# Performance work log

Measured on AMD Instinct MI355X. Metric: run time of the kernel, lower is better.

## Reference

```python
import jax, jax.numpy as jnp
import numpy as np

N_NODES = 50000
N_EDGES = 800000
VOCAB = 1000
EMBED = 128
HIDDEN = 128
N_CLASSES = 10
N_GRAPHS = 64


def setup_inputs() -> dict:
    key = jax.random.key(0)
    ks = jax.random.split(key, 12)
    x_idx = jax.random.randint(ks[0], (N_NODES,), 0, VOCAB)
    edge_index = jax.random.randint(ks[1], (2, N_EDGES), 0, N_NODES)
    batch = jnp.sort(jax.random.randint(ks[2], (N_NODES,), 0, N_GRAPHS))
    s = lambda k, shp, fan: jax.random.normal(k, shp, jnp.float32) / jnp.sqrt(fan)
    return {
        "x_idx": x_idx,
        "edge_index": edge_index,
        "batch": batch,
        "embed_table": jax.random.normal(ks[3], (VOCAB, EMBED), jnp.float32),
        "Wl1": s(ks[4], (HIDDEN, EMBED), EMBED),
        "bl1": jnp.zeros((HIDDEN,), jnp.float32),
        "Wr1": s(ks[5], (HIDDEN, EMBED), EMBED),
        "Wl2": s(ks[6], (HIDDEN, HIDDEN), HIDDEN),
        "bl2": jnp.zeros((HIDDEN,), jnp.float32),
        "Wr2": s(ks[7], (HIDDEN, HIDDEN), HIDDEN),
        "linW": s(ks[8], (N_CLASSES, HIDDEN), HIDDEN),
        "linb": jnp.zeros((N_CLASSES,), jnp.float32),
    }


def _sage_conv(x, src, dst, Wl, bl, Wr):
    # mean aggregation of source features into destination nodes (PyG SAGEConv, aggr='mean')
    msg_sum = jax.ops.segment_sum(x[src], dst, num_segments=N_NODES)  # [N, d]
    cnt = jax.ops.segment_sum(jnp.ones((src.shape[0],), x.dtype), dst, num_segments=N_NODES)
    agg = msg_sum / jnp.maximum(cnt, 1.0)[:, None]
    # out = lin_l(agg) + lin_r(x); lin_l has bias, lin_r has none
    return agg @ Wl.T + bl + x @ Wr.T


def reference(x_idx, edge_index, batch, embed_table, Wl1, bl1, Wr1, Wl2, bl2, Wr2, linW, linb):
    src, dst = edge_index[0], edge_index[1]
    x = embed_table[x_idx]  # [N, EMBED]
    x = jax.nn.relu(_sage_conv(x, src, dst, Wl1, bl1, Wr1))
    x = jax.nn.relu(_sage_conv(x, src, dst, Wl2, bl2, Wr2))
    # global mean pool over graphs
    g_sum = jax.ops.segment_sum(x, batch, num_segments=N_GRAPHS)  # [G, HIDDEN]
    g_cnt = jax.ops.segment_sum(jnp.ones((x.shape[0],), x.dtype), batch, num_segments=N_GRAPHS)
    pooled = g_sum / jnp.maximum(g_cnt, 1.0)[:, None]
    return pooled @ linW.T + linb  # [G, N_CLASSES]
```

## Files before the change

### kernel.cpp

```cpp
#include <hip/hip_runtime.h>

#define N_NODES 50000
#define N_EDGES 800000
#define N_GRAPHS 64
#define SCAN_BLOCKS 196

#define NCHUNK 32
#define CHUNK_E (N_EDGES / NCHUNK)
#define NRANGE 4
#define RSZ (N_NODES / NRANGE)

#define K1_HIST (NCHUNK * NRANGE)
#define K1_EMBED (N_NODES * 16 / 256)
#define K1_PREP 32

#define QDW (N_NODES * 16)
#define QUS (N_NODES * 32)

typedef __bf16 bf16x8 __attribute__((ext_vector_type(8)));
typedef float f32x4 __attribute__((ext_vector_type(4)));

static __device__ __forceinline__ unsigned short f2bf(float f) {
    union { float f; unsigned u; } v; v.f = f;
    unsigned u = v.u;
    u += 0x7fffu + ((u >> 16) & 1u);
    return (unsigned short)(u >> 16);
}
static __device__ __forceinline__ float bf2f(unsigned short h) {
    union { unsigned u; float f; } v; v.u = ((unsigned)h) << 16; return v.f;
}
static __device__ __forceinline__ float bflo(unsigned w) {
    union { unsigned u; float f; } v; v.u = w << 16; return v.f;
}
static __device__ __forceinline__ float bfhi(unsigned w) {
    union { unsigned u; float f; } v; v.u = w & 0xffff0000u; return v.f;
}

__global__ __launch_bounds__(256) void k1_kernel(const int* __restrict__ dst,
                                                 int* __restrict__ part,
                                                 const int* __restrict__ x_idx,
                                                 const float* __restrict__ table,
                                                 unsigned short* __restrict__ X,
                                                 const float* __restrict__ Wl1,
                                                 const float* __restrict__ Wr1,
                                                 const float* __restrict__ Wl2,
                                                 const float* __restrict__ Wr2,
                                                 unsigned short* __restrict__ blob,
                                                 float* __restrict__ gsum) {
    const int b = blockIdx.x;
    if (b < K1_HIST) {
        __shared__ int h[RSZ];
        const int c = b >> 2;
        const int r = b & 3;
        const int rbase = r * RSZ;
        for (int i = threadIdx.x; i < RSZ; i += 256) h[i] = 0;
        __syncthreads();
        const int4* d4 = (const int4*)(dst + c * CHUNK_E);
        for (int i = threadIdx.x; i < CHUNK_E / 4; i += 256) {
            int4 d = d4[i];
            unsigned a;
            a = (unsigned)(d.x - rbase); if (a < RSZ) atomicAdd(&h[a], 1);
            a = (unsigned)(d.y - rbase); if (a < RSZ) atomicAdd(&h[a], 1);
            a = (unsigned)(d.z - rbase); if (a < RSZ) atomicAdd(&h[a], 1);
            a = (unsigned)(d.w - rbase); if (a < RSZ) atomicAdd(&h[a], 1);
        }
        __syncthreads();
        int* p = part + (size_t)c * N_NODES + rbase;
        for (int i = threadIdx.x; i < RSZ; i += 256) p[i] = h[i];
    } else if (b < K1_HIST + K1_EMBED) {
        int i = (b - K1_HIST) * 256 + threadIdx.x;
        int n = i >> 4, cq = i & 15;
        const float4* src = (const float4*)(table + (size_t)x_idx[n] * 128 + cq * 8);
        float4 a = src[0], bb = src[1];
        uint4 o;
        o.x = (unsigned)f2bf(a.x)  | ((unsigned)f2bf(a.y)  << 16);
        o.y = (unsigned)f2bf(a.z)  | ((unsigned)f2bf(a.w)  << 16);
        o.z = (unsigned)f2bf(bb.x) | ((unsigned)f2bf(bb.y) << 16);
        o.w = (unsigned)f2bf(bb.z) | ((unsigned)f2bf(bb.w) << 16);
        int qq = cq >> 2;
        ((uint4*)X)[(size_t)qq * (N_NODES * 4) + n * 4 + (cq & 3)] = o;
    } else {
        int s = (b - K1_HIST - K1_EMBED) * 256 + threadIdx.x;
        gsum[s] = 0.f;
        int g = s >> 12;
        int sl = s & 4095;
        int fidx = sl >> 6, lane = sl & 63;
        int m = fidx >> 5, kk = (fidx >> 3) & 3, tile = fidx & 7;
        const float* W = g ? (m ? Wr2 : Wl2) : (m ? Wr1 : Wl1);
        int n  = tile * 16 + (lane & 15);
        int k0 = kk * 32 + (lane >> 4) * 8;
        const float4* src = (const float4*)(W + n * 128 + k0);
        float4 a = src[0], bb = src[1];
        uint4 o;
        o.x = (unsigned)f2bf(a.x)  | ((unsigned)f2bf(a.y)  << 16);
        o.y = (unsigned)f2bf(a.z)  | ((unsigned)f2bf(a.w)  << 16);
        o.z = (unsigned)f2bf(bb.x) | ((unsigned)f2bf(bb.y) << 16);
        o.w = (unsigned)f2bf(bb.z) | ((unsigned)f2bf(bb.w) << 16);
        ((uint4*)blob)[s] = o;
    }
}

__global__ __launch_bounds__(256) void cntsum_kernel(const int* __restrict__ part,
                                                     int* __restrict__ cnt,
                                                     int* __restrict__ bsum) {
    int t = threadIdx.x;
    int n = blockIdx.x * 256 + t;
    int s = 0;
    if (n < N_NODES) {
#pragma unroll
        for (int c = 0; c < NCHUNK; ++c) s += part[(size_t)c * N_NODES + n];
        cnt[n] = s;
    }
#pragma unroll
    for (int off = 32; off > 0; off >>= 1) s += __shfl_down(s, off, 64);
    __shared__ int ws[4];
    if ((t & 63) == 0) ws[t >> 6] = s;
    __syncthreads();
    if (t == 0) bsum[blockIdx.x] = ws[0] + ws[1] + ws[2] + ws[3];
}

__global__ __launch_bounds__(256) void rowptroff_kernel(const int* __restrict__ cnt,
                                                        const int* __restrict__ bsum,
                                                        const int* __restrict__ part,
                                                        int* __restrict__ rowptr,
                                                        int* __restrict__ off) {
    __shared__ int sb[256];
    __shared__ int sd[256];
    int t = threadIdx.x;
    sb[t] = (t < SCAN_BLOCKS) ? bsum[t] : 0;
    __syncthreads();
    for (int o = 1; o < 256; o <<= 1) {
        int add = (t >= o) ? sb[t - o] : 0;
        __syncthreads();
        sb[t] += add;
        __syncthreads();
    }
    int boff = (blockIdx.x > 0) ? sb[blockIdx.x - 1] : 0;

    int i = blockIdx.x * 256 + t;
    int v = (i < N_NODES) ? cnt[i] : 0;
    sd[t] = v;
    __syncthreads();
    for (int o = 1; o < 256; o <<= 1) {
        int add = (t >= o) ? sd[t - o] : 0;
        __syncthreads();
        sd[t] += add;
        __syncthreads();
    }
    int excl = sd[t] - v + boff;
    if (i < N_NODES) {
        rowptr[i] = excl;
        if (i == N_NODES - 1) rowptr[N_NODES] = excl + v;
        int run = excl;
#pragma unroll
        for (int c = 0; c < NCHUNK; ++c) {
            off[(size_t)c * N_NODES + i] = run;
            run += part[(size_t)c * N_NODES + i];
        }
    }
}

__global__ __launch_bounds__(256) void scatter_kernel(const int* __restrict__ src,
                                                      const int* __restrict__ dst,
                                                      const int* __restrict__ off,
                                                      int* __restrict__ csr) {
    __shared__ int h[RSZ];
    const int c = blockIdx.x >> 2;
    const int r = blockIdx.x & 3;
    const int rbase = r * RSZ;
    const int* o = off + (size_t)c * N_NODES + rbase;
    for (int i = threadIdx.x; i < RSZ; i += 256) h[i] = o[i];
    __syncthreads();
    const int4* d4 = (const int4*)(dst + c * CHUNK_E);
    const int4* s4 = (const int4*)(src + c * CHUNK_E);
    for (int i = threadIdx.x; i < CHUNK_E / 4; i += 256) {
        int4 d = d4[i];
        int4 s = s4[i];
        unsigned a;
        a = (unsigned)(d.x - rbase); if (a < RSZ) csr[atomicAdd(&h[a], 1)] = s.x;
        a = (unsigned)(d.y - rbase); if (a < RSZ) csr[atomicAdd(&h[a], 1)] = s.y;
        a = (unsigned)(d.z - rbase); if (a < RSZ) csr[atomicAdd(&h[a], 1)] = s.z;
        a = (unsigned)(d.w - rbase); if (a < RSZ) csr[atomicAdd(&h[a], 1)] = s.w;
    }
}

__global__ __launch_bounds__(256) void agg_kernel(const unsigned* __restrict__ Xq,
                                                  const int* __restrict__ rowptr,
                                                  const int* __restrict__ csr,
                                                  unsigned* __restrict__ AGGq) {
    const int t = threadIdx.x;
    const int lane = t & 63;
    const int g = lane >> 4;
    const int f = lane & 15;
    const int n = blockIdx.x * 16 + (t >> 6) * 4 + g;
    const unsigned* Xb = Xq + (size_t)blockIdx.y * QDW;
    int beg = rowptr[n], end = rowptr[n + 1];
    float sx = 0.f, sy = 0.f;
    int i = beg;
    for (; i + 4 <= end; i += 4) {
        int s0 = csr[i], s1 = csr[i + 1], s2 = csr[i + 2], s3 = csr[i + 3];
        unsigned v0 = Xb[(size_t)s0 * 16 + f];
        unsigned v1 = Xb[(size_t)s1 * 16 + f];
        unsigned v2 = Xb[(size_t)s2 * 16 + f];
        unsigned v3 = Xb[(size_t)s3 * 16 + f];
        sx += (bflo(v0) + bflo(v1)) + (bflo(v2) + bflo(v3));
        sy += (bfhi(v0) + bfhi(v1)) + (bfhi(v2) + bfhi(v3));
    }
    for (; i < end; ++i) {
        unsigned v = Xb[(size_t)csr[i] * 16 + f];
        sx += bflo(v); sy += bfhi(v);
    }
    float inv = 1.f / (float)max(end - beg, 1);
    AGGq[(size_t)blockIdx.y * QDW + (size_t)n * 16 + f] =
        (unsigned)f2bf(sx * inv) | ((unsigned)f2bf(sy * inv) << 16);
}

__global__ __launch_bounds__(256) void gemm_kernel(const unsigned short* __restrict__ A0,
                                                   const unsigned short* __restrict__ A1,
                                                   const unsigned short* __restrict__ wblob,
                                                   const float* __restrict__ bias,
                                                   unsigned short* __restrict__ Y) {
    __shared__ char lds[65536];
    const int t = threadIdx.x, lane = t & 63, w = t >> 6;
    const int row0 = blockIdx.x * 128 + w * 32;

    {
        const char* src = (const char*)wblob + w * 16384 + lane * 16;
        char* dst = lds + w * 16384;
#pragma unroll
        for (int i = 0; i < 16; ++i) {
            __builtin_amdgcn_global_load_lds(
                (const __attribute__((address_space(1))) unsigned*)(src + i * 1024),
                (__attribute__((address_space(3))) unsigned*)(dst + i * 1024), 16, 0, 0);
        }
    }
    __syncthreads();

    f32x4 acc[2][8];
#pragma unroll
    for (int rt = 0; rt < 2; ++rt)
#pragma unroll
        for (int tl = 0; tl < 8; ++tl) acc[rt][tl] = (f32x4){0.f, 0.f, 0.f, 0.f};

    int rA = min(row0 + (lane & 15),      N_NODES - 1);
    int rB = min(row0 + 16 + (lane & 15), N_NODES - 1);
    const int kl = (lane >> 4) * 8;

#pragma unroll
    for (int km = 0; km < 8; ++km) {
        const unsigned short* Aq = ((km < 4) ? A0 : A1) + (size_t)(km & 3) * QUS;
        bf16x8 a0 = *(const bf16x8*)(Aq + (size_t)rA * 32 + kl);
        bf16x8 a1 = *(const bf16x8*)(Aq + (size_t)rB * 32 + kl);
        const char* bbase = lds + km * 8192 + lane * 16;
#pragma unroll
        for (int tile = 0; tile < 8; ++tile) {
            bf16x8 b = *(const bf16x8*)(bbase + tile * 1024);
            acc[0][tile] = __builtin_amdgcn_mfma_f32_16x16x32_bf16(a0, b, acc[0][tile], 0, 0, 0);
            acc[1][tile] = __builtin_amdgcn_mfma_f32_16x16x32_bf16(a1, b, acc[1][tile], 0, 0, 0);
        }
    }

    const int c     = lane & 15;
    const int rbase = (lane >> 4) * 4;
#pragma unroll
    for (int rt = 0; rt < 2; ++rt) {
#pragma unroll
        for (int tile = 0; tile < 8; ++tile) {
            int col = tile * 16 + c;
            float bv = bias[col];
            int q = col >> 5, wc = col & 31;
#pragma unroll
            for (int j = 0; j < 4; ++j) {
                int r = row0 + rt * 16 + rbase + j;
                if (r < N_NODES)
                    Y[(size_t)q * QUS + (size_t)r * 32 + wc] =
                        f2bf(fmaxf(acc[rt][tile][j] + bv, 0.f));
            }
        }
    }
}

__global__ __launch_bounds__(256) void gemm_pool_kernel(const unsigned short* __restrict__ A0,
                                                        const unsigned short* __restrict__ A1,
                                                        const unsigned short* __restrict__ wblob,
                                                        const float* __restrict__ bias,
                                                        const int* __restrict__ batch,
                                                        float* __restrict__ gsum) {
    __shared__ char lds[65536];
    const int t = threadIdx.x, lane = t & 63, w = t >> 6;
    const int brow0 = blockIdx.x * 128;
    const int row0  = brow0 + w * 32;

    {
        const char* src = (const char*)wblob + w * 16384 + lane * 16;
        char* dst = lds + w * 16384;
#pragma unroll
        for (int i = 0; i < 16; ++i) {
            __builtin_amdgcn_global_load_lds(
                (const __attribute__((address_space(1))) unsigned*)(src + i * 1024),
                (__attribute__((address_space(3))) unsigned*)(dst + i * 1024), 16, 0, 0);
        }
    }
    __syncthreads();

    f32x4 acc[2][8];
#pragma unroll
    for (int rt = 0; rt < 2; ++rt)
#pragma unroll
        for (int tl = 0; tl < 8; ++tl) acc[rt][tl] = (f32x4){0.f, 0.f, 0.f, 0.f};

    int rA = min(row0 + (lane & 15),      N_NODES - 1);
    int rB = min(row0 + 16 + (lane & 15), N_NODES - 1);
    const int kl = (lane >> 4) * 8;

#pragma unroll
    for (int km = 0; km < 8; ++km) {
        const unsigned short* Aq = ((km < 4) ? A0 : A1) + (size_t)(km & 3) * QUS;
        bf16x8 a0 = *(const bf16x8*)(Aq + (size_t)rA * 32 + kl);
        bf16x8 a1 = *(const bf16x8*)(Aq + (size_t)rB * 32 + kl);
        const char* bbase = lds + km * 8192 + lane * 16;
#pragma unroll
        for (int tile = 0; tile < 8; ++tile) {
            bf16x8 b = *(const bf16x8*)(bbase + tile * 1024);
            acc[0][tile] = __builtin_amdgcn_mfma_f32_16x16x32_bf16(a0, b, acc[0][tile], 0, 0, 0);
            acc[1][tile] = __builtin_amdgcn_mfma_f32_16x16x32_bf16(a1, b, acc[1][tile], 0, 0, 0);
        }
    }

    __syncthreads();
    float* ftile = (float*)lds;
    const int c     = lane & 15;
    const int rbase = (lane >> 4) * 4;
#pragma unroll
    for (int rt = 0; rt < 2; ++rt) {
#pragma unroll
        for (int tile = 0; tile < 8; ++tile) {
            int col = tile * 16 + c;
            float bv = bias[col];
#pragma unroll
            for (int j = 0; j < 4; ++j) {
                int lr = w * 32 + rt * 16 + rbase + j;
                ftile[lr * 128 + col] = fmaxf(acc[rt][tile][j] + bv, 0.f);
            }
        }
    }
    __syncthreads();

    const int col  = t & 127;
    const int half = t >> 7;
    float s = 0.f;
    int curg = -1;
    for (int rr = 0; rr < 64; ++rr) {
        int r = brow0 + half * 64 + rr;
        if (r >= N_NODES) break;
        int g = batch[r];
        if (g != curg) {
            if (curg >= 0) atomicAdd(&gsum[curg * 128 + col], s);
            curg = g; s = 0.f;
        }
        s += ftile[(half * 64 + rr) * 128 + col];
    }
    if (curg >= 0) atomicAdd(&gsum[curg * 128 + col], s);
}

__global__ void final_kernel(const float* __restrict__ gsum, const int* __restrict__ batch,
                             const float* __restrict__ linW, const float* __restrict__ linb,
                             float* __restrict__ out) {
    int t = blockIdx.x * 256 + threadIdx.x;
    if (t >= N_GRAPHS * 10) return;
    int g = t / 10, j = t % 10;
    int bnd[2];
    for (int c = 0; c < 2; ++c) {
        int target = g + c;
        int lo = 0, hi = N_NODES;
        while (lo < hi) { int mid = (lo + hi) >> 1; if (batch[mid] < target) lo = mid + 1; else hi = mid; }
        bnd[c] = lo;
    }
    float invc = 1.f / (float)max(bnd[1] - bnd[0], 1);
    float s = 0.f;
    for (int k = 0; k < 128; ++k) s += gsum[g * 128 + k] * linW[j * 128 + k];
    out[t] = linb[j] + s * invc;
}

extern "C" void kernel_launch(void* const* d_in, const int* in_sizes, int n_in,
                              void* d_out, int out_size, void* d_ws, size_t ws_size,
                              hipStream_t stream) {
    const int*   x_idx = (const int*)d_in[0];
    const int*   eidx  = (const int*)d_in[1];
    const int*   batch = (const int*)d_in[2];
    const float* table = (const float*)d_in[3];
    const float* Wl1   = (const float*)d_in[4];
    const float* bl1   = (const float*)d_in[5];
    const float* Wr1   = (const float*)d_in[6];
    const float* Wl2   = (const float*)d_in[7];
    const float* bl2   = (const float*)d_in[8];
    const float* Wr2   = (const float*)d_in[9];
    const float* linW  = (const float*)d_in[10];
    const float* linb  = (const float*)d_in[11];
    float*       out   = (float*)d_out;

    const int* src = eidx;
    const int* dst = eidx + N_EDGES;

    unsigned short* X    = (unsigned short*)d_ws;
    unsigned short* AGG  = X   + (size_t)N_NODES * 128;
    unsigned short* Y1   = AGG + (size_t)N_NODES * 128;
    unsigned short* blob = Y1  + (size_t)N_NODES * 128;
    float* gsum = (float*)(blob + 65536);
    int* cnt    = (int*)(gsum + N_GRAPHS * 128);
    int* rowptr = cnt + N_NODES;
    int* csr    = rowptr + (N_NODES + 1);
    int* bsum   = csr + N_EDGES;
    int* part   = bsum + SCAN_BLOCKS;
    int* off    = part + (size_t)NCHUNK * N_NODES;

    k1_kernel<<<K1_HIST + K1_EMBED + K1_PREP, 256, 0, stream>>>(
        dst, part, x_idx, table, X, Wl1, Wr1, Wl2, Wr2, blob, gsum);
    cntsum_kernel   <<<SCAN_BLOCKS, 256, 0, stream>>>(part, cnt, bsum);
    rowptroff_kernel<<<SCAN_BLOCKS, 256, 0, stream>>>(cnt, bsum, part, rowptr, off);
    scatter_kernel  <<<NCHUNK * NRANGE, 256, 0, stream>>>(src, dst, off, csr);

    agg_kernel <<<dim3(N_NODES / 16, 4), 256, 0, stream>>>((const unsigned*)X, rowptr, csr, (unsigned*)AGG);
    gemm_kernel<<<dim3((N_NODES + 127) / 128), 256, 0, stream>>>(AGG, X, blob, bl1, Y1);
    agg_kernel      <<<dim3(N_NODES / 16, 4), 256, 0, stream>>>((const unsigned*)Y1, rowptr, csr, (unsigned*)AGG);
    gemm_pool_kernel<<<dim3((N_NODES + 127) / 128), 256, 0, stream>>>(AGG, Y1, blob + 32768, bl2, batch, gsum);

    final_kernel<<<3, 256, 0, stream>>>(gsum, batch, linW, linb, out);
}
```

Before: 179.7 us.

## Switch node features from quarter-split layout to row-major with 16-byte gathers

Node feature storage changes from four 32-column quarter planes to plain row-major 128-wide bf16 rows. The aggregation kernel now has 16 lanes gather a full 256-byte row using 16-byte loads per lane, in a single grid pass instead of four. It reads the CSR indices once per node rather than four times, and each gathered row is one contiguous segment. In exchange there are fewer threads in flight and each lane holds more registers and accumulators. The GEMM kernels are adjusted to read and write the new layout.

```diff
diff --git a/kernel.cpp b/kernel.cpp
--- a/kernel.cpp
+++ b/kernel.cpp
@@ -13,9 +13,6 @@
 #define K1_HIST (NCHUNK * NRANGE)
 #define K1_EMBED (N_NODES * 16 / 256)
 #define K1_PREP 32
-
-#define QDW (N_NODES * 16)
-#define QUS (N_NODES * 32)
 
 typedef __bf16 bf16x8 __attribute__((ext_vector_type(8)));
 typedef float f32x4 __attribute__((ext_vector_type(4)));
@@ -25,9 +22,6 @@
     unsigned u = v.u;
     u += 0x7fffu + ((u >> 16) & 1u);
     return (unsigned short)(u >> 16);
-}
-static __device__ __forceinline__ float bf2f(unsigned short h) {
-    union { unsigned u; float f; } v; v.u = ((unsigned)h) << 16; return v.f;
 }
 static __device__ __forceinline__ float bflo(unsigned w) {
     union { unsigned u; float f; } v; v.u = w << 16; return v.f;
@@ -77,8 +71,7 @@
         o.y = (unsigned)f2bf(a.z)  | ((unsigned)f2bf(a.w)  << 16);
         o.z = (unsigned)f2bf(bb.x) | ((unsigned)f2bf(bb.y) << 16);
         o.w = (unsigned)f2bf(bb.z) | ((unsigned)f2bf(bb.w) << 16);
-        int qq = cq >> 2;
-        ((uint4*)X)[(size_t)qq * (N_NODES * 4) + n * 4 + (cq & 3)] = o;
+        ((uint4*)X)[i] = o;
     } else {
         int s = (b - K1_HIST - K1_EMBED) * 256 + threadIdx.x;
         gsum[s] = 0.f;
@@ -184,35 +177,48 @@
     }
 }
 
-__global__ __launch_bounds__(256) void agg_kernel(const unsigned* __restrict__ Xq,
+__global__ __launch_bounds__(256) void agg_kernel(const unsigned short* __restrict__ X,
                                                   const int* __restrict__ rowptr,
                                                   const int* __restrict__ csr,
-                                                  unsigned* __restrict__ AGGq) {
+                                                  unsigned short* __restrict__ AGG) {
     const int t = threadIdx.x;
     const int lane = t & 63;
-    const int g = lane >> 4;
     const int f = lane & 15;
-    const int n = blockIdx.x * 16 + (t >> 6) * 4 + g;
-    const unsigned* Xb = Xq + (size_t)blockIdx.y * QDW;
+    const int n = blockIdx.x * 16 + (t >> 6) * 4 + (lane >> 4);
     int beg = rowptr[n], end = rowptr[n + 1];
-    float sx = 0.f, sy = 0.f;
+    const char* Xb = (const char*)X + f * 16;
+    float a0 = 0.f, a1 = 0.f, a2 = 0.f, a3 = 0.f,
+          a4 = 0.f, a5 = 0.f, a6 = 0.f, a7 = 0.f;
     int i = beg;
     for (; i + 4 <= end; i += 4) {
         int s0 = csr[i], s1 = csr[i + 1], s2 = csr[i + 2], s3 = csr[i + 3];
-        unsigned v0 = Xb[(size_t)s0 * 16 + f];
-        unsigned v1 = Xb[(size_t)s1 * 16 + f];
-        unsigned v2 = Xb[(size_t)s2 * 16 + f];
-        unsigned v3 = Xb[(size_t)s3 * 16 + f];
-        sx += (bflo(v0) + bflo(v1)) + (bflo(v2) + bflo(v3));
-        sy += (bfhi(v0) + bfhi(v1)) + (bfhi(v2) + bfhi(v3));
+        uint4 v0 = *(const uint4*)(Xb + (size_t)s0 * 256);
+        uint4 v1 = *(const uint4*)(Xb + (size_t)s1 * 256);
+        uint4 v2 = *(const uint4*)(Xb + (size_t)s2 * 256);
+        uint4 v3 = *(const uint4*)(Xb + (size_t)s3 * 256);
+        a0 += (bflo(v0.x) + bflo(v1.x)) + (bflo(v2.x) + bflo(v3.x));
+        a1 += (bfhi(v0.x) + bfhi(v1.x)) + (bfhi(v2.x) + bfhi(v3.x));
+        a2 += (bflo(v0.y) + bflo(v1.y)) + (bflo(v2.y) + bflo(v3.y));
+        a3 += (bfhi(v0.y) + bfhi(v1.y)) + (bfhi(v2.y) + bfhi(v3.y));
+        a4 += (bflo(v0.z) + bflo(v1.z)) + (bflo(v2.z) + bflo(v3.z));
+        a5 += (bfhi(v0.z) + bfhi(v1.z)) + (bfhi(v2.z) + bfhi(v3.z));
+        a6 += (bflo(v0.w) + bflo(v1.w)) + (bflo(v2.w) + bflo(v3.w));
+        a7 += (bfhi(v0.w) + bfhi(v1.w)) + (bfhi(v2.w) + bfhi(v3.w));
     }
     for (; i < end; ++i) {
-        unsigned v = Xb[(size_t)csr[i] * 16 + f];
-        sx += bflo(v); sy += bfhi(v);
+        uint4 v0 = *(const uint4*)(Xb + (size_t)csr[i] * 256);
+        a0 += bflo(v0.x); a1 += bfhi(v0.x);
+        a2 += bflo(v0.y); a3 += bfhi(v0.y);
+        a4 += bflo(v0.z); a5 += bfhi(v0.z);
+        a6 += bflo(v0.w); a7 += bfhi(v0.w);
     }
     float inv = 1.f / (float)max(end - beg, 1);
-    AGGq[(size_t)blockIdx.y * QDW + (size_t)n * 16 + f] =
-        (unsigned)f2bf(sx * inv) | ((unsigned)f2bf(sy * inv) << 16);
+    uint4 o;
+    o.x = (unsigned)f2bf(a0 * inv) | ((unsigned)f2bf(a1 * inv) << 16);
+    o.y = (unsigned)f2bf(a2 * inv) | ((unsigned)f2bf(a3 * inv) << 16);
+    o.z = (unsigned)f2bf(a4 * inv) | ((unsigned)f2bf(a5 * inv) << 16);
+    o.w = (unsigned)f2bf(a6 * inv) | ((unsigned)f2bf(a7 * inv) << 16);
+    *(uint4*)((char*)AGG + (size_t)n * 256 + f * 16) = o;
 }
 
 __global__ __launch_bounds__(256) void gemm_kernel(const unsigned short* __restrict__ A0,
@@ -248,9 +254,10 @@
 
 #pragma unroll
     for (int km = 0; km < 8; ++km) {
-        const unsigned short* Aq = ((km < 4) ? A0 : A1) + (size_t)(km & 3) * QUS;
-        bf16x8 a0 = *(const bf16x8*)(Aq + (size_t)rA * 32 + kl);
-        bf16x8 a1 = *(const bf16x8*)(Aq + (size_t)rB * 32 + kl);
+        const unsigned short* A = (km < 4) ? A0 : A1;
+        int k0 = (km & 3) * 32 + kl;
+        bf16x8 a0 = *(const bf16x8*)(A + (size_t)rA * 128 + k0);
+        bf16x8 a1 = *(const bf16x8*)(A + (size_t)rB * 128 + k0);
         const char* bbase = lds + km * 8192 + lane * 16;
 #pragma unroll
         for (int tile = 0; tile < 8; ++tile) {
@@ -268,13 +275,11 @@
         for (int tile = 0; tile < 8; ++tile) {
             int col = tile * 16 + c;
             float bv = bias[col];
-            int q = col >> 5, wc = col & 31;
 #pragma unroll
             for (int j = 0; j < 4; ++j) {
                 int r = row0 + rt * 16 + rbase + j;
                 if (r < N_NODES)
-                    Y[(size_t)q * QUS + (size_t)r * 32 + wc] =
-                        f2bf(fmaxf(acc[rt][tile][j] + bv, 0.f));
+                    Y[(size_t)r * 128 + col] = f2bf(fmaxf(acc[rt][tile][j] + bv, 0.f));
             }
         }
     }
@@ -315,9 +320,10 @@
 
 #pragma unroll
     for (int km = 0; km < 8; ++km) {
-        const unsigned short* Aq = ((km < 4) ? A0 : A1) + (size_t)(km & 3) * QUS;
-        bf16x8 a0 = *(const bf16x8*)(Aq + (size_t)rA * 32 + kl);
-        bf16x8 a1 = *(const bf16x8*)(Aq + (size_t)rB * 32 + kl);
+        const unsigned short* A = (km < 4) ? A0 : A1;
+        int k0 = (km & 3) * 32 + kl;
+        bf16x8 a0 = *(const bf16x8*)(A + (size_t)rA * 128 + k0);
+        bf16x8 a1 = *(const bf16x8*)(A + (size_t)rB * 128 + k0);
         const char* bbase = lds + km * 8192 + lane * 16;
 #pragma unroll
         for (int tile = 0; tile < 8; ++tile) {
@@ -420,9 +426,9 @@
     rowptroff_kernel<<<SCAN_BLOCKS, 256, 0, stream>>>(cnt, bsum, part, rowptr, off);
     scatter_kernel  <<<NCHUNK * NRANGE, 256, 0, stream>>>(src, dst, off, csr);
 
-    agg_kernel <<<dim3(N_NODES / 16, 4), 256, 0, stream>>>((const unsigned*)X, rowptr, csr, (unsigned*)AGG);
+    agg_kernel <<<dim3(N_NODES / 16), 256, 0, stream>>>(X, rowptr, csr, AGG);
     gemm_kernel<<<dim3((N_NODES + 127) / 128), 256, 0, stream>>>(AGG, X, blob, bl1, Y1);
-    agg_kernel      <<<dim3(N_NODES / 16, 4), 256, 0, stream>>>((const unsigned*)Y1, rowptr, csr, (unsigned*)AGG);
+    agg_kernel      <<<dim3(N_NODES / 16), 256, 0, stream>>>(Y1, rowptr, csr, AGG);
     gemm_pool_kernel<<<dim3((N_NODES + 127) / 128), 256, 0, stream>>>(AGG, Y1, blob + 32768, bl2, batch, gsum);
 
     final_kernel<<<3, 256, 0, stream>>>(gsum, batch, linW, linb, out);
```

Result: faster. 153.5 us (-14.6%).

## Fuse neighbor mean aggregation into SAGE GEMM kernels with row-major features

Applied to the files above, without the earlier changes.

Replaces the separate aggregation kernel and GEMM kernel with one templated sage kernel. Each lane gathers its neighbor rows directly into registers and feeds the normalized aggregate straight into the MFMA A operand, so the AGG intermediate is no longer written to and re-read from global memory. The feature layout changes from four quarter-planes to plain row-major 256-byte rows, which allows 16-byte gathers per neighbor. In exchange, the grid drops to about 391 blocks, with each lane walking two full neighbor lists serially. This lowers parallelism and latency hiding for the irregular gather and adds register pressure.

```diff
diff --git a/kernel.cpp b/kernel.cpp
--- a/kernel.cpp
+++ b/kernel.cpp
@@ -14,11 +14,9 @@
 #define K1_EMBED (N_NODES * 16 / 256)
 #define K1_PREP 32
 
-#define QDW (N_NODES * 16)
-#define QUS (N_NODES * 32)
-
 typedef __bf16 bf16x8 __attribute__((ext_vector_type(8)));
 typedef float f32x4 __attribute__((ext_vector_type(4)));
+typedef unsigned uint32x4v __attribute__((ext_vector_type(4)));
 
 static __device__ __forceinline__ unsigned short f2bf(float f) {
     union { float f; unsigned u; } v; v.f = f;
@@ -26,15 +24,18 @@
     u += 0x7fffu + ((u >> 16) & 1u);
     return (unsigned short)(u >> 16);
 }
-static __device__ __forceinline__ float bf2f(unsigned short h) {
-    union { unsigned u; float f; } v; v.u = ((unsigned)h) << 16; return v.f;
-}
 static __device__ __forceinline__ float bflo(unsigned w) {
     union { unsigned u; float f; } v; v.u = w << 16; return v.f;
 }
 static __device__ __forceinline__ float bfhi(unsigned w) {
     union { unsigned u; float f; } v; v.u = w & 0xffff0000u; return v.f;
 }
+
+#define ACC8(A, v) do { \
+    A[0] += bflo((v).x); A[1] += bfhi((v).x); \
+    A[2] += bflo((v).y); A[3] += bfhi((v).y); \
+    A[4] += bflo((v).z); A[5] += bfhi((v).z); \
+    A[6] += bflo((v).w); A[7] += bfhi((v).w); } while (0)
 
 __global__ __launch_bounds__(256) void k1_kernel(const int* __restrict__ dst,
                                                  int* __restrict__ part,
@@ -77,8 +78,7 @@
         o.y = (unsigned)f2bf(a.z)  | ((unsigned)f2bf(a.w)  << 16);
         o.z = (unsigned)f2bf(bb.x) | ((unsigned)f2bf(bb.y) << 16);
         o.w = (unsigned)f2bf(bb.z) | ((unsigned)f2bf(bb.w) << 16);
-        int qq = cq >> 2;
-        ((uint4*)X)[(size_t)qq * (N_NODES * 4) + n * 4 + (cq & 3)] = o;
+        ((uint4*)X)[i] = o;
     } else {
         int s = (b - K1_HIST - K1_EMBED) * 256 + threadIdx.x;
         gsum[s] = 0.f;
@@ -184,56 +184,111 @@
     }
 }
 
-__global__ __launch_bounds__(256) void agg_kernel(const unsigned* __restrict__ Xq,
-                                                  const int* __restrict__ rowptr,
-                                                  const int* __restrict__ csr,
-                                                  unsigned* __restrict__ AGGq) {
-    const int t = threadIdx.x;
-    const int lane = t & 63;
-    const int g = lane >> 4;
-    const int f = lane & 15;
-    const int n = blockIdx.x * 16 + (t >> 6) * 4 + g;
-    const unsigned* Xb = Xq + (size_t)blockIdx.y * QDW;
-    int beg = rowptr[n], end = rowptr[n + 1];
-    float sx = 0.f, sy = 0.f;
-    int i = beg;
-    for (; i + 4 <= end; i += 4) {
-        int s0 = csr[i], s1 = csr[i + 1], s2 = csr[i + 2], s3 = csr[i + 3];
-        unsigned v0 = Xb[(size_t)s0 * 16 + f];
-        unsigned v1 = Xb[(size_t)s1 * 16 + f];
-        unsigned v2 = Xb[(size_t)s2 * 16 + f];
-        unsigned v3 = Xb[(size_t)s3 * 16 + f];
-        sx += (bflo(v0) + bflo(v1)) + (bflo(v2) + bflo(v3));
-        sy += (bfhi(v0) + bfhi(v1)) + (bfhi(v2) + bfhi(v3));
-    }
-    for (; i < end; ++i) {
-        unsigned v = Xb[(size_t)csr[i] * 16 + f];
-        sx += bflo(v); sy += bfhi(v);
-    }
-    float inv = 1.f / (float)max(end - beg, 1);
-    AGGq[(size_t)blockIdx.y * QDW + (size_t)n * 16 + f] =
-        (unsigned)f2bf(sx * inv) | ((unsigned)f2bf(sy * inv) << 16);
-}
-
-__global__ __launch_bounds__(256) void gemm_kernel(const unsigned short* __restrict__ A0,
-                                                   const unsigned short* __restrict__ A1,
+template<int POOL>
+__global__ __launch_bounds__(256) void sage_kernel(const unsigned short* __restrict__ Xf,
+                                                   const int* __restrict__ rowptr,
+                                                   const int* __restrict__ csr,
                                                    const unsigned short* __restrict__ wblob,
                                                    const float* __restrict__ bias,
-                                                   unsigned short* __restrict__ Y) {
+                                                   unsigned short* __restrict__ Y,
+                                                   const int* __restrict__ batch,
+                                                   float* __restrict__ gsum) {
     __shared__ char lds[65536];
     const int t = threadIdx.x, lane = t & 63, w = t >> 6;
-    const int row0 = blockIdx.x * 128 + w * 32;
+    const int brow0 = blockIdx.x * 128;
+    const int row0  = brow0 + w * 32;
+    const int rr = lane & 15;
+    const int jc = lane >> 4;
 
     {
-        const char* src = (const char*)wblob + w * 16384 + lane * 16;
-        char* dst = lds + w * 16384;
+        const char* srcp = (const char*)wblob + w * 16384 + lane * 16;
+        char* dstp = lds + w * 16384;
 #pragma unroll
         for (int i = 0; i < 16; ++i) {
             __builtin_amdgcn_global_load_lds(
-                (const __attribute__((address_space(1))) unsigned*)(src + i * 1024),
-                (__attribute__((address_space(3))) unsigned*)(dst + i * 1024), 16, 0, 0);
-        }
-    }
+                (const __attribute__((address_space(1))) unsigned*)(srcp + i * 1024),
+                (__attribute__((address_space(3))) unsigned*)(dstp + i * 1024), 16, 0, 0);
+        }
+    }
+
+    const int rA = min(row0 + rr,      N_NODES - 1);
+    const int rB = min(row0 + 16 + rr, N_NODES - 1);
+
+    bf16x8 xA[4], xB[4];
+#pragma unroll
+    for (int j = 0; j < 4; ++j) {
+        xA[j] = *(const bf16x8*)((const char*)Xf + (size_t)rA * 256 + j * 64 + jc * 16);
+        xB[j] = *(const bf16x8*)((const char*)Xf + (size_t)rB * 256 + j * 64 + jc * 16);
+    }
+
+    float aA[4][8], aB[4][8];
+#pragma unroll
+    for (int j = 0; j < 4; ++j)
+#pragma unroll
+        for (int e = 0; e < 8; ++e) { aA[j][e] = 0.f; aB[j][e] = 0.f; }
+
+    const int begA = rowptr[rA], endA = rowptr[rA + 1];
+    const int begB = rowptr[rB], endB = rowptr[rB + 1];
+    const char* Xb = (const char*)Xf + jc * 16;
+
+    {
+        int i = begA;
+        for (; i + 2 <= endA; i += 2) {
+            int s0 = csr[i], s1 = csr[i + 1];
+            const char* p0 = Xb + (size_t)s0 * 256;
+            const char* p1 = Xb + (size_t)s1 * 256;
+            uint4 u0 = *(const uint4*)(p0),       u1 = *(const uint4*)(p0 + 64);
+            uint4 u2 = *(const uint4*)(p0 + 128), u3 = *(const uint4*)(p0 + 192);
+            uint4 v0 = *(const uint4*)(p1),       v1 = *(const uint4*)(p1 + 64);
+            uint4 v2 = *(const uint4*)(p1 + 128), v3 = *(const uint4*)(p1 + 192);
+            ACC8(aA[0], u0); ACC8(aA[1], u1); ACC8(aA[2], u2); ACC8(aA[3], u3);
+            ACC8(aA[0], v0); ACC8(aA[1], v1); ACC8(aA[2], v2); ACC8(aA[3], v3);
+        }
+        if (i < endA) {
+            const char* p0 = Xb + (size_t)csr[i] * 256;
+            uint4 u0 = *(const uint4*)(p0),       u1 = *(const uint4*)(p0 + 64);
+            uint4 u2 = *(const uint4*)(p0 + 128), u3 = *(const uint4*)(p0 + 192);
+            ACC8(aA[0], u0); ACC8(aA[1], u1); ACC8(aA[2], u2); ACC8(aA[3], u3);
+        }
+    }
+    {
+        int i = begB;
+        for (; i + 2 <= endB; i += 2) {
+            int s0 = csr[i], s1 = csr[i + 1];
+            const char* p0 = Xb + (size_t)s0 * 256;
+            const char* p1 = Xb + (size_t)s1 * 256;
+            uint4 u0 = *(const uint4*)(p0),       u1 = *(const uint4*)(p0 + 64);
+            uint4 u2 = *(const uint4*)(p0 + 128), u3 = *(const uint4*)(p0 + 192);
+            uint4 v0 = *(const uint4*)(p1),       v1 = *(const uint4*)(p1 + 64);
+            uint4 v2 = *(const uint4*)(p1 + 128), v3 = *(const uint4*)(p1 + 192);
+            ACC8(aB[0], u0); ACC8(aB[1], u1); ACC8(aB[2], u2); ACC8(aB[3], u3);
+            ACC8(aB[0], v0); ACC8(aB[1], v1); ACC8(aB[2], v2); ACC8(aB[3], v3);
+        }
+        if (i < endB) {
+            const char* p0 = Xb + (size_t)csr[i] * 256;
+            uint4 u0 = *(const uint4*)(p0),       u1 = *(const uint4*)(p0 + 64);
+            uint4 u2 = *(const uint4*)(p0 + 128), u3 = *(const uint4*)(p0 + 192);
+            ACC8(aB[0], u0); ACC8(aB[1], u1); ACC8(aB[2], u2); ACC8(aB[3], u3);
+        }
+    }
+
+    const float invA = 1.f / (float)max(endA - begA, 1);
+    const float invB = 1.f / (float)max(endB - begB, 1);
+    bf16x8 fA[4], fB[4];
+#pragma unroll
+    for (int j = 0; j < 4; ++j) {
+        uint32x4v ua, ub;
+#pragma unroll
+        for (int p = 0; p < 4; ++p) {
+            ua[p] = (unsigned)f2bf(aA[j][2 * p] * invA) |
+                    ((unsigned)f2bf(aA[j][2 * p + 1] * invA) << 16);
+            ub[p] = (unsigned)f2bf(aB[j][2 * p] * invB) |
+                    ((unsigned)f2bf(aB[j][2 * p + 1] * invB) << 16);
+        }
+        fA[j] = __builtin_bit_cast(bf16x8, ua);
+        fB[j] = __builtin_bit_cast(bf16x8, ub);
+    }
+
     __syncthreads();
 
     f32x4 acc[2][8];
@@ -242,15 +297,10 @@
 #pragma unroll
         for (int tl = 0; tl < 8; ++tl) acc[rt][tl] = (f32x4){0.f, 0.f, 0.f, 0.f};
 
-    int rA = min(row0 + (lane & 15),      N_NODES - 1);
-    int rB = min(row0 + 16 + (lane & 15), N_NODES - 1);
-    const int kl = (lane >> 4) * 8;
-
 #pragma unroll
     for (int km = 0; km < 8; ++km) {
-        const unsigned short* Aq = ((km < 4) ? A0 : A1) + (size_t)(km & 3) * QUS;
-        bf16x8 a0 = *(const bf16x8*)(Aq + (size_t)rA * 32 + kl);
-        bf16x8 a1 = *(const bf16x8*)(Aq + (size_t)rB * 32 + kl);
+        bf16x8 a0 = (km < 4) ? fA[km] : xA[km - 4];
+        bf16x8 a1 = (km < 4) ? fB[km] : xB[km - 4];
         const char* bbase = lds + km * 8192 + lane * 16;
 #pragma unroll
         for (int tile = 0; tile < 8; ++tile) {
@@ -262,105 +312,54 @@
 
     const int c     = lane & 15;
     const int rbase = (lane >> 4) * 4;
-#pragma unroll
-    for (int rt = 0; rt < 2; ++rt) {
-#pragma unroll
-        for (int tile = 0; tile < 8; ++tile) {
-            int col = tile * 16 + c;
-            float bv = bias[col];
-            int q = col >> 5, wc = col & 31;
-#pragma unroll
-            for (int j = 0; j < 4; ++j) {
-                int r = row0 + rt * 16 + rbase + j;
-                if (r < N_NODES)
-                    Y[(size_t)q * QUS + (size_t)r * 32 + wc] =
-                        f2bf(fmaxf(acc[rt][tile][j] + bv, 0.f));
+    if (POOL == 0) {
+#pragma unroll
+        for (int rt = 0; rt < 2; ++rt) {
+#pragma unroll
+            for (int tile = 0; tile < 8; ++tile) {
+                int col = tile * 16 + c;
+                float bv = bias[col];
+#pragma unroll
+                for (int j = 0; j < 4; ++j) {
+                    int r = row0 + rt * 16 + rbase + j;
+                    if (r < N_NODES)
+                        Y[(size_t)r * 128 + col] = f2bf(fmaxf(acc[rt][tile][j] + bv, 0.f));
+                }
             }
         }
-    }
-}
-
-__global__ __launch_bounds__(256) void gemm_pool_kernel(const unsigned short* __restrict__ A0,
-                                                        const unsigned short* __restrict__ A1,
-                                                        const unsigned short* __restrict__ wblob,
-                                                        const float* __restrict__ bias,
-                                                        const int* __restrict__ batch,
-                                                        float* __restrict__ gsum) {
-    __shared__ char lds[65536];
-    const int t = threadIdx.x, lane = t & 63, w = t >> 6;
-    const int brow0 = blockIdx.x * 128;
-    const int row0  = brow0 + w * 32;
-
-    {
-        const char* src = (const char*)wblob + w * 16384 + lane * 16;
-        char* dst = lds + w * 16384;
-#pragma unroll
-        for (int i = 0; i < 16; ++i) {
-            __builtin_amdgcn_global_load_lds(
-                (const __attribute__((address_space(1))) unsigned*)(src + i * 1024),
-                (__attribute__((address_space(3))) unsigned*)(dst + i * 1024), 16, 0, 0);
-        }
-    }
-    __syncthreads();
-
-    f32x4 acc[2][8];
-#pragma unroll
-    for (int rt = 0; rt < 2; ++rt)
-#pragma unroll
-        for (int tl = 0; tl < 8; ++tl) acc[rt][tl] = (f32x4){0.f, 0.f, 0.f, 0.f};
-
-    int rA = min(row0 + (lane & 15),      N_NODES - 1);
-    int rB = min(row0 + 16 + (lane & 15), N_NODES - 1);
-    const int kl = (lane >> 4) * 8;
-
-#pragma unroll
-    for (int km = 0; km < 8; ++km) {
-        const unsigned short* Aq = ((km < 4) ? A0 : A1) + (size_t)(km & 3) * QUS;
-        bf16x8 a0 = *(const bf16x8*)(Aq + (size_t)rA * 32 + kl);
-        bf16x8 a1 = *(const bf16x8*)(Aq + (size_t)rB * 32 + kl);
-        const char* bbase = lds + km * 8192 + lane * 16;
-#pragma unroll
-        for (int tile = 0; tile < 8; ++tile) {
-            bf16x8 b = *(const bf16x8*)(bbase + tile * 1024);
-            acc[0][tile] = __builtin_amdgcn_mfma_f32_16x16x32_bf16(a0, b, acc[0][tile], 0, 0, 0);
-            acc[1][tile] = __builtin_amdgcn_mfma_f32_16x16x32_bf16(a1, b, acc[1][tile], 0, 0, 0);
-        }
-    }
-
-    __syncthreads();
-    float* ftile = (float*)lds;
-    const int c     = lane & 15;
-    const int rbase = (lane >> 4) * 4;
-#pragma unroll
-    for (int rt = 0; rt < 2; ++rt) {
-#pragma unroll
-        for (int tile = 0; tile < 8; ++tile) {
-            int col = tile * 16 + c;
-            float bv = bias[col];
-#pragma unroll
-            for (int j = 0; j < 4; ++j) {
-                int lr = w * 32 + rt * 16 + rbase + j;
-                ftile[lr * 128 + col] = fmaxf(acc[rt][tile][j] + bv, 0.f);
+    } else {
+        __syncthreads();
+        float* ftile = (float*)lds;
+#pragma unroll
+        for (int rt = 0; rt < 2; ++rt) {
+#pragma unroll
+            for (int tile = 0; tile < 8; ++tile) {
+                int col = tile * 16 + c;
+                float bv = bias[col];
+#pragma unroll
+                for (int j = 0; j < 4; ++j) {
+                    int lr = w * 32 + rt * 16 + rbase + j;
+                    ftile[lr * 128 + col] = fmaxf(acc[rt][tile][j] + bv, 0.f);
+                }
             }
         }
-    }
-    __syncthreads();
-
-    const int col  = t & 127;
-    const int half = t >> 7;
-    float s = 0.f;
-    int curg = -1;
-    for (int rr = 0; rr < 64; ++rr) {
-        int r = brow0 + half * 64 + rr;
-        if (r >= N_NODES) break;
-        int g = batch[r];
-        if (g != curg) {
-            if (curg >= 0) atomicAdd(&gsum[curg * 128 + col], s);
-            curg = g; s = 0.f;
-        }
-        s += ftile[(half * 64 + rr) * 128 + col];
-    }
-    if (curg >= 0) atomicAdd(&gsum[curg * 128 + col], s);
+        __syncthreads();
+        const int col  = t & 127;
+        const int half = t >> 7;
+        float s = 0.f;
+        int curg = -1;
+        for (int rr2 = 0; rr2 < 64; ++rr2) {
+            int r = brow0 + half * 64 + rr2;
+            if (r >= N_NODES) break;
+            int g = batch[r];
+            if (g != curg) {
+                if (curg >= 0) atomicAdd(&gsum[curg * 128 + col], s);
+                curg = g; s = 0.f;
+            }
+            s += ftile[(half * 64 + rr2) * 128 + col];
+        }
+        if (curg >= 0) atomicAdd(&gsum[curg * 128 + col], s);
+    }
 }
 
 __global__ void final_kernel(const float* __restrict__ gsum, const int* __restrict__ batch,
@@ -403,9 +402,8 @@
     const int* dst = eidx + N_EDGES;
 
     unsigned short* X    = (unsigned short*)d_ws;
-    unsigned short* AGG  = X   + (size_t)N_NODES * 128;
-    unsigned short* Y1   = AGG + (size_t)N_NODES * 128;
-    unsigned short* blob = Y1  + (size_t)N_NODES * 128;
+    unsigned short* Y1   = X  + (size_t)N_NODES * 128;
+    unsigned short* blob = Y1 + (size_t)N_NODES * 128;
     float* gsum = (float*)(blob + 65536);
     int* cnt    = (int*)(gsum + N_GRAPHS * 128);
     int* rowptr = cnt + N_NODES;
@@ -420,10 +418,10 @@
     rowptroff_kernel<<<SCAN_BLOCKS, 256, 0, stream>>>(cnt, bsum, part, rowptr, off);
     scatter_kernel  <<<NCHUNK * NRANGE, 256, 0, stream>>>(src, dst, off, csr);
 
-    agg_kernel <<<dim3(N_NODES / 16, 4), 256, 0, stream>>>((const unsigned*)X, rowptr, csr, (unsigned*)AGG);
-    gemm_kernel<<<dim3((N_NODES + 127) / 128), 256, 0, stream>>>(AGG, X, blob, bl1, Y1);
-    agg_kernel      <<<dim3(N_NODES / 16, 4), 256, 0, stream>>>((const unsigned*)Y1, rowptr, csr, (unsigned*)AGG);
-    gemm_pool_kernel<<<dim3((N_NODES + 127) / 128), 256, 0, stream>>>(AGG, Y1, blob + 32768, bl2, batch, gsum);
+    sage_kernel<0><<<dim3((N_NODES + 127) / 128), 256, 0, stream>>>(
+        X, rowptr, csr, blob, bl1, Y1, nullptr, nullptr);
+    sage_kernel<1><<<dim3((N_NODES + 127) / 128), 256, 0, stream>>>(
+        Y1, rowptr, csr, blob + 32768, bl2, nullptr, batch, gsum);
 
     final_kernel<<<3, 256, 0, stream>>>(gsum, batch, linW, linb, out);
 }
```

New measurement: 205.0 us. 1.14x slower.
